# Optimization experiments

Measured on AMD Instinct MI355X. Metric: run time of the kernel, lower is better.

## Reference

```python
import jax, jax.numpy as jnp
import numpy as np

B, T, C = 4, 2048, 1024
H, DK, DV = 16, 64, 64


def setup_inputs() -> dict:
    key = jax.random.key(0)
    ks = jax.random.split(key, 12)
    s = 1.0 / np.sqrt(C)
    inp = {
        "Q": jax.random.normal(ks[0], (B, T, C), jnp.float32),
        "K": jax.random.normal(ks[1], (B, T, C), jnp.float32),
        "V": jax.random.normal(ks[2], (B, T, C), jnp.float32),
        # causal mask: True (==1) means masked out
        "mask": jnp.broadcast_to(jnp.triu(jnp.ones((T, T), bool), k=1), (B, 1, T, T)),
        "Wq": jax.random.uniform(ks[3], (C, H * DK), jnp.float32, -s, s),
        "bq": jax.random.uniform(ks[4], (H * DK,), jnp.float32, -s, s),
        "Wk": jax.random.uniform(ks[5], (C, H * DK), jnp.float32, -s, s),
        "bk": jax.random.uniform(ks[6], (H * DK,), jnp.float32, -s, s),
        "Wv": jax.random.uniform(ks[7], (C, H * DV), jnp.float32, -s, s),
        "bv": jax.random.uniform(ks[8], (H * DV,), jnp.float32, -s, s),
        "Wo": jax.random.uniform(ks[9], (H * DV, C), jnp.float32, -s, s),
        "bo": jax.random.uniform(ks[10], (C,), jnp.float32, -s, s),
    }
    return inp


def _split(x, d):
    b, t, _ = x.shape
    return x.reshape(b, t, H, d).transpose(0, 2, 1, 3)  # (B,H,T,d)


def reference(Q, K, V, mask, Wq, bq, Wk, bk, Wv, bv, Wo, bo):
    Qh = _split(Q @ Wq + bq, DK)
    Kh = _split(K @ Wk + bk, DK)
    Vh = _split(V @ Wv + bv, DV)
    scores = jnp.einsum('bhqd,bhkd->bhqk', Qh, Kh) / jnp.sqrt(jnp.float32(DK))
    scores = jnp.where(mask, -jnp.inf, scores)
    attn = jax.nn.softmax(scores, axis=-1)
    out = jnp.einsum('bhqk,bhkd->bhqd', attn, Vh)
    out = out.transpose(0, 2, 1, 3).reshape(B, T, H * DV)
    return out @ Wo + bo
```

## Files before the change

### kernel.cpp

```cpp
#include <hip/hip_runtime.h>
#include <stdint.h>

#define BATCH 4
#define SEQ   2048
#define CH    1024
#define NH    16
#define HD    64

#define QSCALE 0.18033688011112042f

#define GM 8192
#define GN 1024
#define GK 1024

typedef __attribute__((ext_vector_type(8))) short bf16x8;
typedef __attribute__((ext_vector_type(4))) short bf16x4;
typedef __attribute__((ext_vector_type(4))) float f32x4;

__device__ inline unsigned short f2bf(float f) {
    unsigned u = __float_as_uint(f);
    u += 0x7fff + ((u >> 16) & 1);
    return (unsigned short)(u >> 16);
}

__device__ inline float fast_exp2(float x) {
    float r;
    asm("v_exp_f32 %0, %1" : "=v"(r) : "v"(x));
    return r;
}

__device__ inline unsigned cvt_pk_bf16(float lo, float hi) {
    unsigned r;
    asm("v_cvt_pk_bf16_f32 %0, %1, %2" : "=v"(r) : "v"(lo), "v"(hi));
    return r;
}

#if __has_builtin(__builtin_amdgcn_mfma_f32_16x16x16bf16_1k)
__device__ inline void mfma16(f32x4& c, bf16x4 a, bf16x4 b) {
    c = __builtin_amdgcn_mfma_f32_16x16x16bf16_1k(a, b, c, 0, 0, 0);
}
#else
__device__ inline void mfma16(f32x4& c, bf16x4 a, bf16x4 b) {
    asm volatile("s_nop 2\n\tv_mfma_f32_16x16x16_bf16 %0, %1, %2, %0"
                 : "+v"(c) : "v"(a), "v"(b));
}
#endif

__device__ inline void gld_lds16(const void* g, void* l) {
    __builtin_amdgcn_global_load_lds((const __attribute__((address_space(1))) void*)g,
                                     (__attribute__((address_space(3))) void*)l,
                                     16, 0, 0);
}

__global__ __launch_bounds__(256) void prep_k(
    const float* __restrict__ Wq, const float* __restrict__ Wk,
    const float* __restrict__ Wv, const float* __restrict__ Wo,
    unsigned short* __restrict__ WqT, unsigned short* __restrict__ WkT,
    unsigned short* __restrict__ WvT, unsigned short* __restrict__ WoT)
{
    __shared__ float tile[32][33];
    const int j     = blockIdx.x >> 10;
    const int local = blockIdx.x & 1023;
    const float* W = (j == 0) ? Wq : (j == 1) ? Wk : (j == 2) ? Wv : Wo;
    unsigned short* Wt = (j == 0) ? WqT : (j == 1) ? WkT : (j == 2) ? WvT : WoT;
    const int bx = (local & 31) * 32;
    const int by = (local >> 5) * 32;
    const int tx = threadIdx.x & 31;
    const int ty = threadIdx.x >> 5;
#pragma unroll
    for (int i = 0; i < 32; i += 8)
        tile[ty + i][tx] = W[(size_t)(by + ty + i) * CH + bx + tx];
    __syncthreads();
#pragma unroll
    for (int i = 0; i < 32; i += 8)
        Wt[(size_t)(bx + ty + i) * CH + by + tx] = f2bf(tile[tx][ty + i]);
}

__global__ __launch_bounds__(256, 2)
void qkv_gemm(const float* __restrict__ Qf, const float* __restrict__ Kf,
              const float* __restrict__ Vf,
              const unsigned short* __restrict__ WqT, const unsigned short* __restrict__ WkT,
              const unsigned short* __restrict__ WvT,
              const float* __restrict__ bq, const float* __restrict__ bk,
              const float* __restrict__ bv,
              unsigned short* __restrict__ Qhb, unsigned short* __restrict__ Khb,
              unsigned short* __restrict__ Vtb)
{
    __shared__ float          As32[128 * 64];
    __shared__ unsigned short Bs[128 * 64];
    const int job = blockIdx.y;
    const float* A32          = (job == 0) ? Qf  : (job == 1) ? Kf  : Vf;
    const unsigned short* Bt  = (job == 0) ? WqT : (job == 1) ? WkT : WvT;
    const float* bias         = (job == 0) ? bq  : (job == 1) ? bk  : bv;
    unsigned short* outp      = (job == 0) ? Qhb : (job == 1) ? Khb : Vtb;
    const float oscale        = (job == 0) ? QSCALE : 1.0f;

    const int tid  = threadIdx.x;
    const int lane = tid & 63;
    const int w    = tid >> 6;
    const int nbn  = GN >> 7;
    const int nbm  = GM >> 7;
    const int xcd  = blockIdx.x & 7;
    const int idx  = blockIdx.x >> 3;
    const int mb   = xcd * (nbm >> 3) + idx / nbn;
    const int nb   = idx % nbn;
    const int m0   = mb << 7;
    const int n0   = nb << 7;
    const int wrow = (w >> 1) << 6;
    const int wcol = (w & 1) << 6;
    const int lr   = lane & 15;
    const int lg   = lane >> 4;

    f32x4 acc[4][4] = {};

    for (int k0 = 0; k0 < GK; k0 += 64) {
#pragma unroll
        for (int i = 0; i < 8; ++i) {
            int chunk = i * 256 + tid;
            int row  = chunk >> 4;
            int l    = (chunk & 15) ^ (row & 15);
            gld_lds16(A32 + (size_t)(m0 + row) * GK + k0 + l * 4,
                      (char*)As32 + chunk * 16);
        }
#pragma unroll
        for (int i = 0; i < 4; ++i) {
            int chunk = i * 256 + tid;
            int row = chunk >> 3;
            int c8  = (chunk & 7) << 3;
            gld_lds16(Bt + (size_t)(n0 + row) * GK + k0 + c8, (char*)Bs + chunk * 16);
        }
        __syncthreads();
#pragma unroll
        for (int kk = 0; kk < 2; ++kk) {
            const int plo = ((kk << 3) | (lg << 1)) ^ lr;
            const int phi = plo ^ 1;
            bf16x8 af[4], bfr[4];
#pragma unroll
            for (int f = 0; f < 4; ++f) {
                const float* base = As32 + (wrow + f * 16 + lr) * 64;
                f32x4 lo = *(const f32x4*)(base + plo * 4);
                f32x4 hi = *(const f32x4*)(base + phi * 4);
                union { bf16x8 v; unsigned u[4]; } cv;
                cv.u[0] = cvt_pk_bf16(lo[0], lo[1]);
                cv.u[1] = cvt_pk_bf16(lo[2], lo[3]);
                cv.u[2] = cvt_pk_bf16(hi[0], hi[1]);
                cv.u[3] = cvt_pk_bf16(hi[2], hi[3]);
                af[f] = cv.v;
            }
#pragma unroll
            for (int f = 0; f < 4; ++f)
                bfr[f] = *(const bf16x8*)(Bs + (wcol + f * 16 + lr) * 64 + kk * 32 + lg * 8);
#pragma unroll
            for (int i = 0; i < 4; ++i)
#pragma unroll
                for (int j = 0; j < 4; ++j)
                    acc[i][j] = __builtin_amdgcn_mfma_f32_16x16x32_bf16(af[i], bfr[j], acc[i][j], 0, 0, 0);
        }
        __syncthreads();
    }

    float bvals[4];
#pragma unroll
    for (int j = 0; j < 4; ++j) bvals[j] = bias[n0 + wcol + j * 16 + lr];

    if (job < 2) {
#pragma unroll
        for (int i = 0; i < 4; ++i) {
            const int mbase = m0 + wrow + i * 16 + lg * 4;
#pragma unroll
            for (int j = 0; j < 4; ++j) {
                const int n = n0 + wcol + j * 16 + lr;
                const int h = n >> 6, d = n & 63;
#pragma unroll
                for (int r = 0; r < 4; ++r) {
                    const int m = mbase + r;
                    const int b = m >> 11, t = m & 2047;
                    outp[((size_t)(b * NH + h) * SEQ + t) * HD + d] = f2bf((acc[i][j][r] + bvals[j]) * oscale);
                }
            }
        }
    } else {
#pragma unroll
        for (int i = 0; i < 4; ++i) {
            const int mbase = m0 + wrow + i * 16 + lg * 4;
#pragma unroll
            for (int j = 0; j < 4; ++j) {
                const int n = n0 + wcol + j * 16 + lr;
                const int h = n >> 6, d = n & 63;
                const int b = mbase >> 11, t = mbase & 2047;
                union { unsigned short s[4]; uint2 v; } pk;
#pragma unroll
                for (int r = 0; r < 4; ++r) pk.s[r] = f2bf(acc[i][j][r] + bvals[j]);
                *(uint2*)(outp + ((size_t)(b * NH + h) * HD + d) * SEQ + t) = pk.v;
            }
        }
    }
}

__global__ __launch_bounds__(256, 2)
void gemm_out(const unsigned short* __restrict__ A,
              const unsigned short* __restrict__ Bt,
              const float* __restrict__ bias,
              float* __restrict__ out)
{
    __shared__ unsigned short As[128 * 64];
    __shared__ unsigned short Bs[128 * 64];
    const int tid  = threadIdx.x;
    const int lane = tid & 63;
    const int w    = tid >> 6;
    const int nbn  = GN >> 7;
    const int nbm  = GM >> 7;
    const int xcd  = blockIdx.x & 7;
    const int idx  = blockIdx.x >> 3;
    const int mb   = xcd * (nbm >> 3) + idx / nbn;
    const int nb   = idx % nbn;
    const int m0   = mb << 7;
    const int n0   = nb << 7;
    const int wrow = (w >> 1) << 6;
    const int wcol = (w & 1) << 6;
    const int lr   = lane & 15;
    const int lg   = lane >> 4;

    f32x4 acc[4][4] = {};

    for (int k0 = 0; k0 < GK; k0 += 64) {
#pragma unroll
        for (int i = 0; i < 4; ++i) {
            int chunk = i * 256 + tid;
            int row = chunk >> 3;
            int c8  = (chunk & 7) << 3;
            gld_lds16(A  + (size_t)(m0 + row) * GK + k0 + c8, (char*)As + chunk * 16);
            gld_lds16(Bt + (size_t)(n0 + row) * GK + k0 + c8, (char*)Bs + chunk * 16);
        }
        __syncthreads();
#pragma unroll
        for (int kk = 0; kk < 2; ++kk) {
            bf16x8 af[4], bfr[4];
#pragma unroll
            for (int f = 0; f < 4; ++f)
                af[f] = *(const bf16x8*)(As + (wrow + f * 16 + lr) * 64 + kk * 32 + lg * 8);
#pragma unroll
            for (int f = 0; f < 4; ++f)
                bfr[f] = *(const bf16x8*)(Bs + (wcol + f * 16 + lr) * 64 + kk * 32 + lg * 8);
#pragma unroll
            for (int i = 0; i < 4; ++i)
#pragma unroll
                for (int j = 0; j < 4; ++j)
                    acc[i][j] = __builtin_amdgcn_mfma_f32_16x16x32_bf16(af[i], bfr[j], acc[i][j], 0, 0, 0);
        }
        __syncthreads();
    }

    float bvals[4];
#pragma unroll
    for (int j = 0; j < 4; ++j) bvals[j] = bias[n0 + wcol + j * 16 + lr];

#pragma unroll
    for (int i = 0; i < 4; ++i) {
        const int mbase = m0 + wrow + i * 16 + lg * 4;
#pragma unroll
        for (int j = 0; j < 4; ++j) {
            const int n = n0 + wcol + j * 16 + lr;
#pragma unroll
            for (int r = 0; r < 4; ++r)
                out[(size_t)(mbase + r) * GN + n] = acc[i][j][r] + bvals[j];
        }
    }
}

__global__ __launch_bounds__(256, 4)
void attn_k(const unsigned short* __restrict__ Qh,
            const unsigned short* __restrict__ Kh,
            const unsigned short* __restrict__ Vt,
            unsigned short* __restrict__ O) {
    __shared__ unsigned short Ks[2][64 * 64];
    __shared__ unsigned short Vs[2][64 * 64];
    const int bh    = blockIdx.x;
    const int qtile = 31 - blockIdx.y;
    const int q0    = qtile << 6;
    const int tid  = threadIdx.x;
    const int lane = tid & 63;
    const int w    = tid >> 6;
    const int lr   = lane & 15;
    const int lg   = lane >> 4;
    const int qw   = q0 + w * 16;

    bf16x4 ones4;
#pragma unroll
    for (int j = 0; j < 4; ++j) ones4[j] = (short)0x3F80;

    bf16x8 qf[2];
#pragma unroll
    for (int kk = 0; kk < 2; ++kk)
        qf[kk] = *(const bf16x8*)(Qh + ((size_t)bh * SEQ + qw + lr) * HD + kk * 32 + lg * 8);

    float mrun = -3e38f;
    f32x4 ot[4] = {};
    f32x4 osum = {};

    const int nkt = qtile + 1;

#define STAGE(KT, B) do {                                                          \
        const int kv_ = (KT) << 6;                                                 \
        _Pragma("unroll")                                                          \
        for (int i_ = 0; i_ < 2; ++i_) {                                           \
            int c_ = i_ * 256 + tid;                                               \
            int row_ = c_ >> 3;                                                    \
            int sk_ = (((c_ & 7) ^ (row_ & 7)) << 3);                              \
            int sv_ = (((c_ & 7) ^ ((row_ >> 1) & 7)) << 3);                       \
            gld_lds16(Kh + ((size_t)bh * SEQ + kv_ + row_) * HD + sk_,             \
                      (char*)Ks[B] + c_ * 16);                                     \
            gld_lds16(Vt + ((size_t)bh * HD + row_) * SEQ + kv_ + sv_,             \
                      (char*)Vs[B] + c_ * 16);                                     \
        }                                                                          \
    } while (0)

    STAGE(0, 0);
    __syncthreads();

    for (int kt = 0; kt < nkt; ++kt) {
        if (kt + 1 < nkt) STAGE(kt + 1, (kt + 1) & 1);
        const unsigned short* Kc = Ks[kt & 1];
        const unsigned short* Vc = Vs[kt & 1];
        const int kv0 = kt << 6;

        f32x4 s[4] = {};
#pragma unroll
        for (int kk = 0; kk < 2; ++kk) {
            const int u = (((kk << 2) | lg) ^ (lr & 7)) << 3;
#pragma unroll
            for (int f = 0; f < 4; ++f) {
                bf16x8 kb = *(const bf16x8*)(Kc + (f * 16 + lr) * 64 + u);
                s[f] = __builtin_amdgcn_mfma_f32_16x16x32_bf16(kb, qf[kk], s[f], 0, 0, 0);
            }
        }

        float rmax = -3e38f;
        if (kv0 + 63 <= qw) {
#pragma unroll
            for (int f = 0; f < 4; ++f)
#pragma unroll
                for (int r = 0; r < 4; ++r) rmax = fmaxf(rmax, s[f][r]);
        } else {
            const int q = qw + lr;
#pragma unroll
            for (int f = 0; f < 4; ++f)
#pragma unroll
                for (int r = 0; r < 4; ++r) {
                    const int kv = kv0 + f * 16 + lg * 4 + r;
                    float v = (kv > q) ? -3e38f : s[f][r];
                    s[f][r] = v;
                    rmax = fmaxf(rmax, v);
                }
        }
        rmax = fmaxf(rmax, __shfl_xor(rmax, 16));
        rmax = fmaxf(rmax, __shfl_xor(rmax, 32));

        if (__any(rmax > mrun)) {
            float mn = fmaxf(mrun, rmax);
            float c  = fast_exp2(mrun - mn);
            mrun = mn;
            osum *= c;
#pragma unroll
            for (int dd = 0; dd < 4; ++dd) ot[dd] *= c;
        }

#pragma unroll
        for (int f = 0; f < 4; ++f) {
#pragma unroll
            for (int r = 0; r < 4; ++r)
                s[f][r] = fast_exp2(s[f][r] - mrun);
            union { bf16x4 v; unsigned u[2]; } pb;
            pb.u[0] = cvt_pk_bf16(s[f][0], s[f][1]);
            pb.u[1] = cvt_pk_bf16(s[f][2], s[f][3]);
            mfma16(osum, ones4, pb.v);
#pragma unroll
            for (int dd = 0; dd < 4; ++dd) {
                const int vcol = ((((f << 1) | (lg >> 1)) ^ (lr >> 1)) << 3) | ((lg & 1) << 2);
                bf16x4 va = *(const bf16x4*)(Vc + (dd * 16 + lr) * 64 + vcol);
                mfma16(ot[dd], va, pb.v);
            }
        }
        __syncthreads();
    }
#undef STAGE

    const int b = bh >> 4, h = bh & 15;
    const float inv = 1.0f / osum[0];
    const int t = qw + lr;
#pragma unroll
    for (int dd = 0; dd < 4; ++dd) {
        union { unsigned short s4[4]; uint2 v; } pk;
#pragma unroll
        for (int r = 0; r < 4; ++r) pk.s4[r] = f2bf(ot[dd][r] * inv);
        *(uint2*)(O + ((size_t)b * SEQ + t) * CH + h * HD + dd * 16 + lg * 4) = pk.v;
    }
}

extern "C" void kernel_launch(void* const* d_in, const int* in_sizes, int n_in,
                              void* d_out, int out_size, void* d_ws, size_t ws_size,
                              hipStream_t stream) {
    const float* Q  = (const float*)d_in[0];
    const float* K  = (const float*)d_in[1];
    const float* V  = (const float*)d_in[2];
    const float* Wq = (const float*)d_in[4];
    const float* bq = (const float*)d_in[5];
    const float* Wk = (const float*)d_in[6];
    const float* bk = (const float*)d_in[7];
    const float* Wv = (const float*)d_in[8];
    const float* bv = (const float*)d_in[9];
    const float* Wo = (const float*)d_in[10];
    const float* bo = (const float*)d_in[11];
    float* out = (float*)d_out;

    const size_t SZ_ACT = (size_t)BATCH * SEQ * CH;
    const size_t SZ_W   = (size_t)CH * CH;

    char* p = (char*)d_ws;
    unsigned short* WqT = (unsigned short*)p; p += SZ_W * 2;
    unsigned short* WkT = (unsigned short*)p; p += SZ_W * 2;
    unsigned short* WvT = (unsigned short*)p; p += SZ_W * 2;
    unsigned short* WoT = (unsigned short*)p; p += SZ_W * 2;
    unsigned short* Qhb = (unsigned short*)p; p += SZ_ACT * 2;
    unsigned short* Khb = (unsigned short*)p; p += SZ_ACT * 2;
    unsigned short* Vtb = (unsigned short*)p; p += SZ_ACT * 2;
    unsigned short* Ob  = (unsigned short*)p; p += SZ_ACT * 2;

    prep_k<<<4096, 256, 0, stream>>>(Wq, Wk, Wv, Wo, WqT, WkT, WvT, WoT);

    qkv_gemm<<<dim3((GM / 128) * (GN / 128), 3), 256, 0, stream>>>(
        Q, K, V, WqT, WkT, WvT, bq, bk, bv, Qhb, Khb, Vtb);

    attn_k<<<dim3(BATCH * NH, SEQ / 64), 256, 0, stream>>>(Qhb, Khb, Vtb, Ob);

    gemm_out<<<(GM / 128) * (GN / 128), 256, 0, stream>>>(Ob, WoT, bo, out);
}
```

Measured before the change: 182.2 us.

## Process two 16-row query subtiles per wave in attention to reuse K/V tiles

The attention kernel now handles 128 query rows per block instead of 64. Each wave carries two 16-row query subtiles with their own online-softmax state, and skips subtiles that lie fully above the causal diagonal. Each K/V tile staged into LDS therefore serves twice as many queries, halving global K/V traffic and staging/sync overhead per query. In exchange the grid is halved (1024 blocks), register pressure rises with the doubled accumulators, and the diagonal tiles leave some waves idle.

```diff
diff --git a/kernel.cpp b/kernel.cpp
--- a/kernel.cpp
+++ b/kernel.cpp
@@ -276,29 +276,31 @@
     __shared__ unsigned short Ks[2][64 * 64];
     __shared__ unsigned short Vs[2][64 * 64];
     const int bh    = blockIdx.x;
-    const int qtile = 31 - blockIdx.y;
-    const int q0    = qtile << 6;
+    const int qtile = 15 - blockIdx.y;
+    const int q0    = qtile << 7;
     const int tid  = threadIdx.x;
     const int lane = tid & 63;
     const int w    = tid >> 6;
     const int lr   = lane & 15;
     const int lg   = lane >> 4;
-    const int qw   = q0 + w * 16;
+    const int qw   = q0 + w * 32;
 
     bf16x4 ones4;
 #pragma unroll
     for (int j = 0; j < 4; ++j) ones4[j] = (short)0x3F80;
 
-    bf16x8 qf[2];
-#pragma unroll
-    for (int kk = 0; kk < 2; ++kk)
-        qf[kk] = *(const bf16x8*)(Qh + ((size_t)bh * SEQ + qw + lr) * HD + kk * 32 + lg * 8);
-
-    float mrun = -3e38f;
-    f32x4 ot[4] = {};
-    f32x4 osum = {};
-
-    const int nkt = qtile + 1;
+    bf16x8 qf[2][2];
+#pragma unroll
+    for (int qi = 0; qi < 2; ++qi)
+#pragma unroll
+        for (int kk = 0; kk < 2; ++kk)
+            qf[qi][kk] = *(const bf16x8*)(Qh + ((size_t)bh * SEQ + qw + qi * 16 + lr) * HD + kk * 32 + lg * 8);
+
+    float mrun[2] = {-3e38f, -3e38f};
+    f32x4 ot[2][4] = {};
+    f32x4 osum[2] = {};
+
+    const int nkt = 2 * qtile + 2;
 
 #define STAGE(KT, B) do {                                                          \
         const int kv_ = (KT) << 6;                                                 \
@@ -324,61 +326,66 @@
         const unsigned short* Vc = Vs[kt & 1];
         const int kv0 = kt << 6;
 
-        f32x4 s[4] = {};
-#pragma unroll
-        for (int kk = 0; kk < 2; ++kk) {
-            const int u = (((kk << 2) | lg) ^ (lr & 7)) << 3;
+#pragma unroll
+        for (int qi = 0; qi < 2; ++qi) {
+            if (kv0 > qw + qi * 16 + 15) continue;
+
+            f32x4 s[4] = {};
+#pragma unroll
+            for (int kk = 0; kk < 2; ++kk) {
+                const int u = (((kk << 2) | lg) ^ (lr & 7)) << 3;
+#pragma unroll
+                for (int f = 0; f < 4; ++f) {
+                    bf16x8 kb = *(const bf16x8*)(Kc + (f * 16 + lr) * 64 + u);
+                    s[f] = __builtin_amdgcn_mfma_f32_16x16x32_bf16(kb, qf[qi][kk], s[f], 0, 0, 0);
+                }
+            }
+
+            float rmax = -3e38f;
+            if (kv0 + 63 <= qw + qi * 16) {
+#pragma unroll
+                for (int f = 0; f < 4; ++f)
+#pragma unroll
+                    for (int r = 0; r < 4; ++r) rmax = fmaxf(rmax, s[f][r]);
+            } else {
+                const int q = qw + qi * 16 + lr;
+#pragma unroll
+                for (int f = 0; f < 4; ++f)
+#pragma unroll
+                    for (int r = 0; r < 4; ++r) {
+                        const int kv = kv0 + f * 16 + lg * 4 + r;
+                        float v = (kv > q) ? -3e38f : s[f][r];
+                        s[f][r] = v;
+                        rmax = fmaxf(rmax, v);
+                    }
+            }
+            rmax = fmaxf(rmax, __shfl_xor(rmax, 16));
+            rmax = fmaxf(rmax, __shfl_xor(rmax, 32));
+
+            if (__any(rmax > mrun[qi])) {
+                float mn = fmaxf(mrun[qi], rmax);
+                float c  = fast_exp2(mrun[qi] - mn);
+                mrun[qi] = mn;
+                osum[qi] *= c;
+#pragma unroll
+                for (int dd = 0; dd < 4; ++dd) ot[qi][dd] *= c;
+            }
+
 #pragma unroll
             for (int f = 0; f < 4; ++f) {
-                bf16x8 kb = *(const bf16x8*)(Kc + (f * 16 + lr) * 64 + u);
-                s[f] = __builtin_amdgcn_mfma_f32_16x16x32_bf16(kb, qf[kk], s[f], 0, 0, 0);
-            }
-        }
-
-        float rmax = -3e38f;
-        if (kv0 + 63 <= qw) {
-#pragma unroll
-            for (int f = 0; f < 4; ++f)
-#pragma unroll
-                for (int r = 0; r < 4; ++r) rmax = fmaxf(rmax, s[f][r]);
-        } else {
-            const int q = qw + lr;
-#pragma unroll
-            for (int f = 0; f < 4; ++f)
-#pragma unroll
-                for (int r = 0; r < 4; ++r) {
-                    const int kv = kv0 + f * 16 + lg * 4 + r;
-                    float v = (kv > q) ? -3e38f : s[f][r];
-                    s[f][r] = v;
-                    rmax = fmaxf(rmax, v);
+#pragma unroll
+                for (int r = 0; r < 4; ++r)
+                    s[f][r] = fast_exp2(s[f][r] - mrun[qi]);
+                union { bf16x4 v; unsigned u[2]; } pb;
+                pb.u[0] = cvt_pk_bf16(s[f][0], s[f][1]);
+                pb.u[1] = cvt_pk_bf16(s[f][2], s[f][3]);
+                mfma16(osum[qi], ones4, pb.v);
+#pragma unroll
+                for (int dd = 0; dd < 4; ++dd) {
+                    const int vcol = ((((f << 1) | (lg >> 1)) ^ (lr >> 1)) << 3) | ((lg & 1) << 2);
+                    bf16x4 va = *(const bf16x4*)(Vc + (dd * 16 + lr) * 64 + vcol);
+                    mfma16(ot[qi][dd], va, pb.v);
                 }
-        }
-        rmax = fmaxf(rmax, __shfl_xor(rmax, 16));
-        rmax = fmaxf(rmax, __shfl_xor(rmax, 32));
-
-        if (__any(rmax > mrun)) {
-            float mn = fmaxf(mrun, rmax);
-            float c  = fast_exp2(mrun - mn);
-            mrun = mn;
-            osum *= c;
-#pragma unroll
-            for (int dd = 0; dd < 4; ++dd) ot[dd] *= c;
-        }
-
-#pragma unroll
-        for (int f = 0; f < 4; ++f) {
-#pragma unroll
-            for (int r = 0; r < 4; ++r)
-                s[f][r] = fast_exp2(s[f][r] - mrun);
-            union { bf16x4 v; unsigned u[2]; } pb;
-            pb.u[0] = cvt_pk_bf16(s[f][0], s[f][1]);
-            pb.u[1] = cvt_pk_bf16(s[f][2], s[f][3]);
-            mfma16(osum, ones4, pb.v);
-#pragma unroll
-            for (int dd = 0; dd < 4; ++dd) {
-                const int vcol = ((((f << 1) | (lg >> 1)) ^ (lr >> 1)) << 3) | ((lg & 1) << 2);
-                bf16x4 va = *(const bf16x4*)(Vc + (dd * 16 + lr) * 64 + vcol);
-                mfma16(ot[dd], va, pb.v);
             }
         }
         __syncthreads();
@@ -386,14 +393,17 @@
 #undef STAGE
 
     const int b = bh >> 4, h = bh & 15;
-    const float inv = 1.0f / osum[0];
-    const int t = qw + lr;
-#pragma unroll
-    for (int dd = 0; dd < 4; ++dd) {
-        union { unsigned short s4[4]; uint2 v; } pk;
-#pragma unroll
-        for (int r = 0; r < 4; ++r) pk.s4[r] = f2bf(ot[dd][r] * inv);
-        *(uint2*)(O + ((size_t)b * SEQ + t) * CH + h * HD + dd * 16 + lg * 4) = pk.v;
+#pragma unroll
+    for (int qi = 0; qi < 2; ++qi) {
+        const float inv = 1.0f / osum[qi][0];
+        const int t = qw + qi * 16 + lr;
+#pragma unroll
+        for (int dd = 0; dd < 4; ++dd) {
+            union { unsigned short s4[4]; uint2 v; } pk;
+#pragma unroll
+            for (int r = 0; r < 4; ++r) pk.s4[r] = f2bf(ot[qi][dd][r] * inv);
+            *(uint2*)(O + ((size_t)b * SEQ + t) * CH + h * HD + dd * 16 + lg * 4) = pk.v;
+        }
     }
 }
 
@@ -431,7 +441,7 @@
     qkv_gemm<<<dim3((GM / 128) * (GN / 128), 3), 256, 0, stream>>>(
         Q, K, V, WqT, WkT, WvT, bq, bk, bv, Qhb, Khb, Vtb);
 
-    attn_k<<<dim3(BATCH * NH, SEQ / 64), 256, 0, stream>>>(Qhb, Khb, Vtb, Ob);
+    attn_k<<<dim3(BATCH * NH, SEQ / 128), 256, 0, stream>>>(Qhb, Khb, Vtb, Ob);
 
     gemm_out<<<(GM / 128) * (GN / 128), 256, 0, stream>>>(Ob, WoT, bo, out);
 }
```

Result: slower. 186.2 us (+2.2%).
